# Kernel tuning notes

Hardware: AMD Instinct MI355X
Metric: run time of the kernel (lower is better)

The kernel has to match this reference:

```python
import jax, jax.numpy as jnp
import numpy as np
from jax import lax

B, T, H, DEPTH = 32, 2048, 256, 4  # batch, max seq len, hidden, num dilated layers


def setup_inputs() -> dict:
    key = jax.random.key(0)
    k0, k1, k2, k3, k4 = jax.random.split(key, 5)
    x = jax.random.normal(k0, (B, T, H), dtype=jnp.float32)
    # ragged lengths in [T//2, T]
    seq_lens = jax.random.randint(k1, (B,), T // 2, T + 1)
    s = 1.0 / np.sqrt(H)
    Wx = jax.random.uniform(k2, (DEPTH, H, H), jnp.float32, -s, s)
    Wh = jax.random.uniform(k3, (DEPTH, H, H), jnp.float32, -s, s)
    b = jax.random.uniform(k4, (DEPTH, H), jnp.float32, -s, s)
    return {"x": x, "Wx": Wx, "Wh": Wh, "b": b, "seq_lens": seq_lens}


def _dilated_layer(x, Wx, Wh, b, dilation):
    # x: [B, T, H]; recurrence h_k = tanh(x_k @ Wx + h_{k-dilation} @ Wh + b),
    # h_prev = 0 for k < dilation. Positions k mod dilation == r form an
    # independent stream, so reshape into `dilation` interleaved streams and
    # run one scan of length ceil(T/dilation).
    Bn, Tn, Hn = x.shape
    pad = (-Tn) % dilation
    xp = jnp.pad(x, ((0, 0), (0, pad), (0, 0)))
    steps = xp.shape[1] // dilation
    # [steps, B, dilation, H]; element [t, b, r] is timestep t*dilation + r
    xs = jnp.transpose(xp.reshape(Bn, steps, dilation, Hn), (1, 0, 2, 3))
    h0 = jnp.zeros((Bn, dilation, Hn), x.dtype)  # init_state per stream

    def step(h, xt):
        h_new = jnp.tanh(xt @ Wx + h @ Wh + b)
        return h_new, h_new

    _, ys = lax.scan(step, h0, xs)  # [steps, B, dilation, H]
    ys = jnp.transpose(ys, (1, 0, 2, 3)).reshape(Bn, steps * dilation, Hn)
    return ys[:, :Tn]


def reference(x, Wx, Wh, b, seq_lens):
    # Mirrors DilatedRNN.forward: output[i][j][k] for depth j with link_len 2**j.
    # Invalid positions (k >= seq_len) never feed into valid ones (forward-only
    # dilated dependence), so we compute densely and mask at the end.
    depth = Wx.shape[0]
    h = x
    outs = []
    for j in range(depth):
        h = _dilated_layer(h, Wx[j], Wh[j], b[j], 2 ** j)
        outs.append(h)
    out = jnp.stack(outs, axis=1)  # [B, depth, T, H] == output TensorArray
    mask = (jnp.arange(out.shape[2])[None, :] < seq_lens[:, None]).astype(x.dtype)
    return out * mask[:, None, :, None]
```

## Files before the change

kernel.cpp:

```cpp
#include <hip/hip_runtime.h>

#define Bn 32
#define Tn 2048
#define Hn 256
#define DEPTHn 4

typedef _Float16 h2 __attribute__((ext_vector_type(2)));
typedef _Float16 h8 __attribute__((ext_vector_type(8)));

__device__ __forceinline__ h2 pkrtz(float a, float b) {
    return __builtin_bit_cast(h2, __builtin_amdgcn_cvt_pkrtz(a, b));
}

#define GR 64
__global__ __launch_bounds__(256, 2) void gemm_xw(
    const float* __restrict__ in, long in_bstride,
    const float* __restrict__ Wx, const float* __restrict__ bias,
    float* __restrict__ Z)
{
    __shared__ __align__(16) float a_lds[GR][264];

    const int tid = threadIdx.x;
    const int row0 = blockIdx.x * GR;

    #pragma unroll
    for (int q = 0; q < 16; ++q) {
        int f = tid + q * 256;
        int r  = f >> 6;
        int c4 = f & 63;
        int grow = row0 + r;
        int b = grow >> 11;
        int t = grow & (Tn - 1);
        float4 v = *(const float4*)(in + (long)b * in_bstride + (long)t * Hn + c4 * 4);
        *(float4*)(&a_lds[r][c4 * 4]) = v;
    }
    __syncthreads();

    const int g  = tid >> 5;
    const int cg = tid & 31;

    float acc[8][8];
    #pragma unroll
    for (int i = 0; i < 8; ++i)
        #pragma unroll
        for (int j = 0; j < 8; ++j) acc[i][j] = 0.f;

    for (int k4 = 0; k4 < 64; ++k4) {
        float4 w[4][2];
        #pragma unroll
        for (int kk = 0; kk < 4; ++kk) {
            const float* wr = Wx + (long)(k4 * 4 + kk) * Hn + cg * 8;
            w[kk][0] = *(const float4*)(wr);
            w[kk][1] = *(const float4*)(wr + 4);
        }
        float4 a[8];
        #pragma unroll
        for (int i = 0; i < 8; ++i)
            a[i] = *(const float4*)(&a_lds[i * 8 + g][k4 * 4]);

        #pragma unroll
        for (int i = 0; i < 8; ++i) {
            #pragma unroll
            for (int kk = 0; kk < 4; ++kk) {
                float av = ((const float*)&a[i])[kk];
                acc[i][0] = fmaf(av, w[kk][0].x, acc[i][0]);
                acc[i][1] = fmaf(av, w[kk][0].y, acc[i][1]);
                acc[i][2] = fmaf(av, w[kk][0].z, acc[i][2]);
                acc[i][3] = fmaf(av, w[kk][0].w, acc[i][3]);
                acc[i][4] = fmaf(av, w[kk][1].x, acc[i][4]);
                acc[i][5] = fmaf(av, w[kk][1].y, acc[i][5]);
                acc[i][6] = fmaf(av, w[kk][1].z, acc[i][6]);
                acc[i][7] = fmaf(av, w[kk][1].w, acc[i][7]);
            }
        }
    }

    float4 b0 = *(const float4*)(bias + cg * 8);
    float4 b1 = *(const float4*)(bias + cg * 8 + 4);
    #pragma unroll
    for (int i = 0; i < 8; ++i) {
        long row = row0 + i * 8 + g;
        float4 o0 = { acc[i][0] + b0.x, acc[i][1] + b0.y, acc[i][2] + b0.z, acc[i][3] + b0.w };
        float4 o1 = { acc[i][4] + b1.x, acc[i][5] + b1.y, acc[i][6] + b1.z, acc[i][7] + b1.w };
        *(float4*)(Z + row * Hn + cg * 8)     = o0;
        *(float4*)(Z + row * Hn + cg * 8 + 4) = o1;
    }
}

__global__ __launch_bounds__(1024, 4) void rnn_layer(
    const float* __restrict__ Z,
    const float* __restrict__ Wh,
    float* __restrict__ out,
    const int* __restrict__ seq_lens,
    int dilation)
{
    __shared__ __align__(16) h2 hbuf[2 * 144];

    const int tid  = threadIdx.x;
    const int wv   = tid >> 6;
    const int lane = tid & 63;
    const int q    = lane >> 4;
    const int c    = lane & 15;
    const int ch   = wv * 16 + c;

    const int s = blockIdx.x;
    const int b = s / dilation;
    const int r = s % dilation;

    h2 w16[32];
    #pragma unroll
    for (int p = 0; p < 32; ++p) {
        float w0 = Wh[(long)(64 * q + 2 * p)     * Hn + ch];
        float w1 = Wh[(long)(64 * q + 2 * p + 1) * Hn + ch];
        w16[p] = pkrtz(w0, w1);
    }

    if (tid < 288) ((unsigned int*)hbuf)[tid] = 0u;
    const int L = seq_lens[b];
    __syncthreads();

    const float* zb = Z + (long)b * Tn * Hn;
    float* ob = out + (long)b * (DEPTHn * Tn * Hn);

    int cur = 0;
    float z_next = zb[(long)r * Hn + ch];
    for (int t = r; t < Tn; t += dilation) {
        float zc = z_next;
        int tn = t + dilation;
        if (tn < Tn) z_next = zb[(long)tn * Hn + ch];

        const h2* hp = &hbuf[cur * 144 + q * 36];
        float a0 = 0.f, a1 = 0.f, a2 = 0.f, a3 = 0.f;
        #pragma unroll
        for (int i4 = 0; i4 < 8; ++i4) {
            h8 hv = *(const h8*)(hp + i4 * 4);
            h2 p0 = __builtin_shufflevector(hv, hv, 0, 1);
            h2 p1 = __builtin_shufflevector(hv, hv, 2, 3);
            h2 p2 = __builtin_shufflevector(hv, hv, 4, 5);
            h2 p3 = __builtin_shufflevector(hv, hv, 6, 7);
            a0 = __builtin_amdgcn_fdot2(p0, w16[i4 * 4 + 0], a0, false);
            a1 = __builtin_amdgcn_fdot2(p1, w16[i4 * 4 + 1], a1, false);
            a2 = __builtin_amdgcn_fdot2(p2, w16[i4 * 4 + 2], a2, false);
            a3 = __builtin_amdgcn_fdot2(p3, w16[i4 * 4 + 3], a3, false);
        }
        float p = (a0 + a1) + (a2 + a3);
        p += __shfl_xor(p, 16);
        p += __shfl_xor(p, 32);

        float ssum = p + zc;
        float e = __expf(2.f * ssum);
        float hn = 1.f - 2.f / (e + 1.f);

        float ho = __shfl_xor(hn, 1);
        if (q == 0) {
            ob[(long)t * Hn + ch] = (t < L) ? hn : 0.f;
            if (!(c & 1)) {
                int m = wv * 8 + (c >> 1);
                hbuf[(cur ^ 1) * 144 + (m >> 5) * 36 + (m & 31)] = pkrtz(hn, ho);
            }
        }
        __syncthreads();
        cur ^= 1;
    }
}

extern "C" void kernel_launch(void* const* d_in, const int* in_sizes, int n_in,
                              void* d_out, int out_size, void* d_ws, size_t ws_size,
                              hipStream_t stream) {
    const float* x    = (const float*)d_in[0];
    const float* Wx   = (const float*)d_in[1];
    const float* Wh   = (const float*)d_in[2];
    const float* bias = (const float*)d_in[3];
    const int*   seq  = (const int*)  d_in[4];
    float* out = (float*)d_out;
    float* Z   = (float*)d_ws;

    for (int j = 0; j < DEPTHn; ++j) {
        const float* in;
        long bstride;
        if (j == 0) { in = x;                             bstride = (long)Tn * Hn; }
        else        { in = out + (long)(j - 1) * Tn * Hn; bstride = (long)DEPTHn * Tn * Hn; }

        hipLaunchKernelGGL(gemm_xw, dim3(Bn * Tn / GR), dim3(256), 0, stream,
                           in, bstride, Wx + (long)j * Hn * Hn, bias + (long)j * Hn, Z);

        int d = 1 << j;
        hipLaunchKernelGGL(rnn_layer, dim3(Bn * d), dim3(1024), 0, stream,
                           Z, Wh + (long)j * Hn * Hn, out + (long)j * Tn * Hn, seq, d);
    }
}
```

Measured before the change: 3.104 ms.

## Halve RNN block size with two channels per lane and DPP quad reductions

The recurrent kernel now runs 512 threads per block instead of 1024, and each lane computes dot products for two output channels. The k-split moves from the lane's high bits to its low two bits, so the cross-lane sum uses quad-permute DPP instead of shfl_xor, and the z prefetch is two steps deep. The barrier is a raw s_waitcnt plus s_barrier, and each producer lane writes its own fp16 half directly, which removes the extra shuffle. The aim is to cut per-step barrier and shuffle latency on the serial recurrence path, at the cost of twice the weight registers per lane.

```diff
diff --git a/kernel.cpp b/kernel.cpp
--- a/kernel.cpp
+++ b/kernel.cpp
@@ -10,6 +10,13 @@
 
 __device__ __forceinline__ h2 pkrtz(float a, float b) {
     return __builtin_bit_cast(h2, __builtin_amdgcn_cvt_pkrtz(a, b));
+}
+
+template <int CTRL>
+__device__ __forceinline__ float dpp_qp(float x) {
+    int xi = __builtin_bit_cast(int, x);
+    int r = __builtin_amdgcn_update_dpp(0, xi, CTRL, 0xF, 0xF, true);
+    return __builtin_bit_cast(float, r);
 }
 
 #define GR 64
@@ -87,7 +94,7 @@
     }
 }
 
-__global__ __launch_bounds__(1024, 4) void rnn_layer(
+__global__ __launch_bounds__(512) void rnn_layer(
     const float* __restrict__ Z,
     const float* __restrict__ Wh,
     float* __restrict__ out,
@@ -99,20 +106,21 @@
     const int tid  = threadIdx.x;
     const int wv   = tid >> 6;
     const int lane = tid & 63;
-    const int q    = lane >> 4;
-    const int c    = lane & 15;
-    const int ch   = wv * 16 + c;
+    const int q    = lane & 3;
+    const int c    = lane >> 2;
+    const int ch0  = wv * 32 + c;
+    const int ch1  = ch0 + 16;
 
     const int s = blockIdx.x;
     const int b = s / dilation;
     const int r = s % dilation;
 
-    h2 w16[32];
+    h2 wA[32], wB[32];
     #pragma unroll
     for (int p = 0; p < 32; ++p) {
-        float w0 = Wh[(long)(64 * q + 2 * p)     * Hn + ch];
-        float w1 = Wh[(long)(64 * q + 2 * p + 1) * Hn + ch];
-        w16[p] = pkrtz(w0, w1);
+        int k0 = 64 * q + 2 * p;
+        wA[p] = pkrtz(Wh[(long)k0 * Hn + ch0], Wh[(long)(k0 + 1) * Hn + ch0]);
+        wB[p] = pkrtz(Wh[(long)k0 * Hn + ch1], Wh[(long)(k0 + 1) * Hn + ch1]);
     }
 
     if (tid < 288) ((unsigned int*)hbuf)[tid] = 0u;
@@ -122,15 +130,25 @@
     const float* zb = Z + (long)b * Tn * Hn;
     float* ob = out + (long)b * (DEPTHn * Tn * Hn);
 
+    const int och = (q & 1) ? ch1 : ch0;
+    const bool producer = (q < 2);
+
     int cur = 0;
-    float z_next = zb[(long)r * Hn + ch];
+    float z1 = 0.f, z2 = 0.f;
+    if (producer) {
+        z1 = zb[(long)r * Hn + och];
+        if (r + dilation < Tn) z2 = zb[(long)(r + dilation) * Hn + och];
+    }
+
     for (int t = r; t < Tn; t += dilation) {
-        float zc = z_next;
-        int tn = t + dilation;
-        if (tn < Tn) z_next = zb[(long)tn * Hn + ch];
+        float zc = z1;
+        z1 = z2;
+        int t2 = t + 2 * dilation;
+        if (producer && t2 < Tn) z2 = zb[(long)t2 * Hn + och];
 
         const h2* hp = &hbuf[cur * 144 + q * 36];
         float a0 = 0.f, a1 = 0.f, a2 = 0.f, a3 = 0.f;
+        float b0 = 0.f, b1 = 0.f, b2 = 0.f, b3 = 0.f;
         #pragma unroll
         for (int i4 = 0; i4 < 8; ++i4) {
             h8 hv = *(const h8*)(hp + i4 * 4);
@@ -138,28 +156,34 @@
             h2 p1 = __builtin_shufflevector(hv, hv, 2, 3);
             h2 p2 = __builtin_shufflevector(hv, hv, 4, 5);
             h2 p3 = __builtin_shufflevector(hv, hv, 6, 7);
-            a0 = __builtin_amdgcn_fdot2(p0, w16[i4 * 4 + 0], a0, false);
-            a1 = __builtin_amdgcn_fdot2(p1, w16[i4 * 4 + 1], a1, false);
-            a2 = __builtin_amdgcn_fdot2(p2, w16[i4 * 4 + 2], a2, false);
-            a3 = __builtin_amdgcn_fdot2(p3, w16[i4 * 4 + 3], a3, false);
-        }
-        float p = (a0 + a1) + (a2 + a3);
-        p += __shfl_xor(p, 16);
-        p += __shfl_xor(p, 32);
-
-        float ssum = p + zc;
-        float e = __expf(2.f * ssum);
-        float hn = 1.f - 2.f / (e + 1.f);
-
-        float ho = __shfl_xor(hn, 1);
-        if (q == 0) {
-            ob[(long)t * Hn + ch] = (t < L) ? hn : 0.f;
-            if (!(c & 1)) {
-                int m = wv * 8 + (c >> 1);
-                hbuf[(cur ^ 1) * 144 + (m >> 5) * 36 + (m & 31)] = pkrtz(hn, ho);
-            }
-        }
-        __syncthreads();
+            a0 = __builtin_amdgcn_fdot2(p0, wA[i4 * 4 + 0], a0, false);
+            a1 = __builtin_amdgcn_fdot2(p1, wA[i4 * 4 + 1], a1, false);
+            a2 = __builtin_amdgcn_fdot2(p2, wA[i4 * 4 + 2], a2, false);
+            a3 = __builtin_amdgcn_fdot2(p3, wA[i4 * 4 + 3], a3, false);
+            b0 = __builtin_amdgcn_fdot2(p0, wB[i4 * 4 + 0], b0, false);
+            b1 = __builtin_amdgcn_fdot2(p1, wB[i4 * 4 + 1], b1, false);
+            b2 = __builtin_amdgcn_fdot2(p2, wB[i4 * 4 + 2], b2, false);
+            b3 = __builtin_amdgcn_fdot2(p3, wB[i4 * 4 + 3], b3, false);
+        }
+        float pA = (a0 + a1) + (a2 + a3);
+        float pB = (b0 + b1) + (b2 + b3);
+
+        pA += dpp_qp<0xB1>(pA);
+        pA += dpp_qp<0x4E>(pA);
+        pB += dpp_qp<0xB1>(pB);
+        pB += dpp_qp<0x4E>(pB);
+
+        if (producer) {
+            float ssum = ((q & 1) ? pB : pA) + zc;
+            float e = __expf(2.f * ssum);
+            float hn = 1.f - 2.f / (e + 1.f);
+            ob[(long)t * Hn + och] = (t < L) ? hn : 0.f;
+            int m = och >> 1;
+            _Float16* hw = (_Float16*)&hbuf[(cur ^ 1) * 144 + (m >> 5) * 36 + (m & 31)];
+            hw[och & 1] = (_Float16)hn;
+        }
+
+        asm volatile("s_waitcnt lgkmcnt(0)\n\ts_barrier" ::: "memory");
         cur ^= 1;
     }
 }
@@ -185,7 +209,7 @@
                            in, bstride, Wx + (long)j * Hn * Hn, bias + (long)j * Hn, Z);
 
         int d = 1 << j;
-        hipLaunchKernelGGL(rnn_layer, dim3(Bn * d), dim3(1024), 0, stream,
+        hipLaunchKernelGGL(rnn_layer, dim3(Bn * d), dim3(512), 0, stream,
                            Z, Wh + (long)j * Hn * Hn, out + (long)j * Tn * Hn, seq, d);
     }
 }
```

After: 2.615 ms. -15.8%, faster.

## Use MFMA for recurrent matvec with 4-wave blocks and deeper Z prefetch

Applied to the files above, without the earlier changes.

The recurrent h@Wh product moves from packed fp16 dot2 instructions on 1024-thread blocks to 16x16x32 f16 MFMA on 256-thread blocks. Wh stays resident in registers as MFMA B fragments. The hidden state is stored as plain fp16 in LDS and broadcast as the A operand, and only row 0 of each MFMA result is used. Z loads are now prefetched two steps ahead, and the barrier becomes a hand-written waitcnt+s_barrier, with the goal of shortening the per-step critical path and its synchronisation cost. The catch is that 15/16 of the MFMA work is wasted, and MFMA latency now sits on the serial chain.

```diff
diff --git a/kernel.cpp b/kernel.cpp
--- a/kernel.cpp
+++ b/kernel.cpp
@@ -5,11 +5,13 @@
 #define Hn 256
 #define DEPTHn 4
 
-typedef _Float16 h2 __attribute__((ext_vector_type(2)));
+typedef unsigned short u16;
+typedef u16    us8 __attribute__((ext_vector_type(8)));
 typedef _Float16 h8 __attribute__((ext_vector_type(8)));
-
-__device__ __forceinline__ h2 pkrtz(float a, float b) {
-    return __builtin_bit_cast(h2, __builtin_amdgcn_cvt_pkrtz(a, b));
+typedef float  f4  __attribute__((ext_vector_type(4)));
+
+__device__ __forceinline__ u16 f2h(float x) {
+    return __builtin_bit_cast(u16, (_Float16)x);
 }
 
 #define GR 64
@@ -87,35 +89,39 @@
     }
 }
 
-__global__ __launch_bounds__(1024, 4) void rnn_layer(
+__global__ __launch_bounds__(256) void rnn_layer(
     const float* __restrict__ Z,
     const float* __restrict__ Wh,
     float* __restrict__ out,
     const int* __restrict__ seq_lens,
     int dilation)
 {
-    __shared__ __align__(16) h2 hbuf[2 * 144];
+    __shared__ __align__(16) u16 hb[2][256];
 
     const int tid  = threadIdx.x;
     const int wv   = tid >> 6;
     const int lane = tid & 63;
-    const int q    = lane >> 4;
+    const int g    = lane >> 4;
     const int c    = lane & 15;
-    const int ch   = wv * 16 + c;
 
     const int s = blockIdx.x;
     const int b = s / dilation;
     const int r = s % dilation;
 
-    h2 w16[32];
-    #pragma unroll
-    for (int p = 0; p < 32; ++p) {
-        float w0 = Wh[(long)(64 * q + 2 * p)     * Hn + ch];
-        float w1 = Wh[(long)(64 * q + 2 * p + 1) * Hn + ch];
-        w16[p] = pkrtz(w0, w1);
-    }
-
-    if (tid < 288) ((unsigned int*)hbuf)[tid] = 0u;
+    us8 Bf[4][8];
+    #pragma unroll
+    for (int j = 0; j < 4; ++j) {
+        #pragma unroll
+        for (int cc = 0; cc < 8; ++cc) {
+            const float* wp = Wh + (long)(32 * cc + 8 * g) * Hn + (64 * wv + 16 * j + c);
+            us8 v;
+            #pragma unroll
+            for (int i = 0; i < 8; ++i) v[i] = f2h(wp[(long)i * Hn]);
+            Bf[j][cc] = v;
+        }
+    }
+
+    hb[0][tid] = 0;
     const int L = seq_lens[b];
     __syncthreads();
 
@@ -123,43 +129,56 @@
     float* ob = out + (long)b * (DEPTHn * Tn * Hn);
 
     int cur = 0;
-    float z_next = zb[(long)r * Hn + ch];
+    float z1[4], z2[4];
+    if (g == 0) {
+        #pragma unroll
+        for (int j = 0; j < 4; ++j) {
+            int ch = 64 * wv + 16 * j + c;
+            z1[j] = zb[(long)r * Hn + ch];
+            z2[j] = (r + dilation < Tn) ? zb[(long)(r + dilation) * Hn + ch] : 0.f;
+        }
+    }
+
     for (int t = r; t < Tn; t += dilation) {
-        float zc = z_next;
-        int tn = t + dilation;
-        if (tn < Tn) z_next = zb[(long)tn * Hn + ch];
-
-        const h2* hp = &hbuf[cur * 144 + q * 36];
-        float a0 = 0.f, a1 = 0.f, a2 = 0.f, a3 = 0.f;
-        #pragma unroll
-        for (int i4 = 0; i4 < 8; ++i4) {
-            h8 hv = *(const h8*)(hp + i4 * 4);
-            h2 p0 = __builtin_shufflevector(hv, hv, 0, 1);
-            h2 p1 = __builtin_shufflevector(hv, hv, 2, 3);
-            h2 p2 = __builtin_shufflevector(hv, hv, 4, 5);
-            h2 p3 = __builtin_shufflevector(hv, hv, 6, 7);
-            a0 = __builtin_amdgcn_fdot2(p0, w16[i4 * 4 + 0], a0, false);
-            a1 = __builtin_amdgcn_fdot2(p1, w16[i4 * 4 + 1], a1, false);
-            a2 = __builtin_amdgcn_fdot2(p2, w16[i4 * 4 + 2], a2, false);
-            a3 = __builtin_amdgcn_fdot2(p3, w16[i4 * 4 + 3], a3, false);
-        }
-        float p = (a0 + a1) + (a2 + a3);
-        p += __shfl_xor(p, 16);
-        p += __shfl_xor(p, 32);
-
-        float ssum = p + zc;
-        float e = __expf(2.f * ssum);
-        float hn = 1.f - 2.f / (e + 1.f);
-
-        float ho = __shfl_xor(hn, 1);
-        if (q == 0) {
-            ob[(long)t * Hn + ch] = (t < L) ? hn : 0.f;
-            if (!(c & 1)) {
-                int m = wv * 8 + (c >> 1);
-                hbuf[(cur ^ 1) * 144 + (m >> 5) * 36 + (m & 31)] = pkrtz(hn, ho);
+        float zc[4];
+        #pragma unroll
+        for (int j = 0; j < 4; ++j) { zc[j] = z1[j]; z1[j] = z2[j]; }
+        int t2 = t + 2 * dilation;
+        if (g == 0 && t2 < Tn) {
+            #pragma unroll
+            for (int j = 0; j < 4; ++j)
+                z2[j] = zb[(long)t2 * Hn + 64 * wv + 16 * j + c];
+        }
+
+        const u16* hp = hb[cur];
+        f4 zero = { 0.f, 0.f, 0.f, 0.f };
+        f4 acc[4][2];
+        #pragma unroll
+        for (int j = 0; j < 4; ++j) { acc[j][0] = zero; acc[j][1] = zero; }
+
+        #pragma unroll
+        for (int cc = 0; cc < 8; ++cc) {
+            us8 av_ = *(const us8*)(hp + 32 * cc + 8 * g);
+            h8 av = __builtin_bit_cast(h8, av_);
+            #pragma unroll
+            for (int j = 0; j < 4; ++j)
+                acc[j][cc & 1] = __builtin_amdgcn_mfma_f32_16x16x32_f16(
+                    av, __builtin_bit_cast(h8, Bf[j][cc]), acc[j][cc & 1], 0, 0, 0);
+        }
+
+        if (g == 0) {
+            #pragma unroll
+            for (int j = 0; j < 4; ++j) {
+                float y = acc[j][0][0] + acc[j][1][0] + zc[j];
+                float e = __expf(2.f * y);
+                float hn = 1.f - 2.f / (e + 1.f);
+                int ch = 64 * wv + 16 * j + c;
+                ob[(long)t * Hn + ch] = (t < L) ? hn : 0.f;
+                hb[cur ^ 1][ch] = f2h(hn);
             }
         }
-        __syncthreads();
+
+        asm volatile("s_waitcnt lgkmcnt(0)\n\ts_barrier" ::: "memory");
         cur ^= 1;
     }
 }
@@ -185,7 +204,7 @@
                            in, bstride, Wx + (long)j * Hn * Hn, bias + (long)j * Hn, Z);
 
         int d = 1 << j;
-        hipLaunchKernelGGL(rnn_layer, dim3(Bn * d), dim3(1024), 0, stream,
+        hipLaunchKernelGGL(rnn_layer, dim3(Bn * d), dim3(256), 0, stream,
                            Z, Wh + (long)j * Hn * Hn, out + (long)j * Tn * Hn, seq, d);
     }
 }
```

Result: slower. 3.196 ms (+3.0%).
